# Kernel optimization log

Hardware: AMD Instinct MI355X
Metric: run time of the kernel (lower is better)

## Reference

```python
import jax, jax.numpy as jnp
import numpy as np

BN_EPS = 1e-5


def setup_inputs() -> dict:
    key = jax.random.key(0)
    ks = jax.random.split(key, 12)
    B, N, G, D = 16, 8192, 64, 384
    C_IN = D + 64 + 3  # 451
    inp = {
        "features": jax.random.normal(ks[0], (B, G, D), jnp.float32),
        "centers": jax.random.normal(ks[1], (B, G, 3), jnp.float32),
        "pc": jax.random.normal(ks[2], (B, N, 3), jnp.float32),
        "category": jax.random.randint(ks[3], (B,), 0, 16, jnp.int64),
        "cat_embed": jax.random.normal(ks[4], (16, 64), jnp.float32) * 0.02,
        "w1": jax.random.normal(ks[5], (256, C_IN), jnp.float32) * (1.0 / np.sqrt(C_IN)),
        "b1": jnp.zeros((256,), jnp.float32),
        "g1": jnp.ones((256,), jnp.float32),
        "be1": jnp.zeros((256,), jnp.float32),
        "m1": jnp.zeros((256,), jnp.float32),
        "v1": jnp.ones((256,), jnp.float32),
        "w2": jax.random.normal(ks[6], (256, 256), jnp.float32) * (1.0 / 16.0),
        "b2": jnp.zeros((256,), jnp.float32),
        "g2": jnp.ones((256,), jnp.float32),
        "be2": jnp.zeros((256,), jnp.float32),
        "m2": jnp.zeros((256,), jnp.float32),
        "v2": jnp.ones((256,), jnp.float32),
        "w3": jax.random.normal(ks[7], (50, 256), jnp.float32) * (1.0 / 16.0),
        "b3": jnp.zeros((50,), jnp.float32),
    }
    return inp


def _bn(x, g, be, m, v):  # x: [B, N, C], inference-mode BatchNorm1d
    return (x - m) * (g * jax.lax.rsqrt(v + BN_EPS)) + be


def reference(features, centers, pc, category, cat_embed,
              w1, b1, g1, be1, m1, v1,
              w2, b2, g2, be2, m2, v2,
              w3, b3):
    B, N, _ = pc.shape
    # Euclidean cdist via norm expansion: [B, N, G]
    p2 = jnp.sum(pc * pc, axis=-1, keepdims=True)            # [B,N,1]
    c2 = jnp.sum(centers * centers, axis=-1)[:, None, :]     # [B,1,G]
    dot = jnp.einsum('bnd,bgd->bng', pc, centers)
    dist = jnp.sqrt(jnp.clip(p2 + c2 - 2.0 * dot, 1e-12))
    # top-3 smallest
    neg_d, knn_idx = jax.lax.top_k(-dist, 3)                 # [B,N,3]
    knn_dist = -neg_d
    w = 1.0 / (knn_dist + 1e-8)
    w = w / jnp.sum(w, axis=-1, keepdims=True)               # [B,N,3]
    # gather per-batch: features [B,G,D], knn_idx [B,N,3] -> [B,N,3,D]
    knn_features = jax.vmap(lambda f, i: f[i])(features, knn_idx)
    point_features = jnp.einsum('bnkd,bnk->bnd', knn_features, w)  # [B,N,D]
    cat_feat = jnp.broadcast_to(cat_embed[category][:, None, :], (B, N, 64))
    combined = jnp.concatenate([point_features, cat_feat, pc], axis=-1)  # [B,N,451]
    # Conv1d(k=1) == per-point dense layer; keep [B,N,C] layout
    h = jnp.einsum('bnc,oc->bno', combined, w1) + b1
    h = jax.nn.relu(_bn(h, g1, be1, m1, v1))
    h = jnp.einsum('bnc,oc->bno', h, w2) + b2
    h = jax.nn.relu(_bn(h, g2, be2, m2, v2))
    seg_logits = jnp.einsum('bnc,oc->bno', h, w3) + b3       # [B,N,50]
    return seg_logits
```

## Files before the change

### kernel.cpp

```cpp
#include <hip/hip_runtime.h>

#define TPB 256

typedef unsigned short u16;
typedef unsigned int u32;
typedef short short8 __attribute__((ext_vector_type(8)));
typedef float f32x4 __attribute__((ext_vector_type(4)));

#define KEEP(x) asm volatile("" :: "v"(x))
#define PIN(x)  asm volatile("" : "+v"(x))

__device__ __forceinline__ u16 f2bf(float x) {
  union { float f; u32 u; } v;
  v.f = x;
  u32 r = v.u + 0x7FFFu + ((v.u >> 16) & 1u);
  return (u16)(r >> 16);
}

__device__ __forceinline__ float bf2f(u16 x) {
  union { u32 u; float f; } v;
  v.u = ((u32)x) << 16;
  return v.f;
}

__global__ void prep_kernel(const float* __restrict__ w1, const float* __restrict__ b1,
                            const float* __restrict__ g1, const float* __restrict__ be1,
                            const float* __restrict__ m1, const float* __restrict__ v1,
                            const float* __restrict__ w2, const float* __restrict__ b2,
                            const float* __restrict__ g2, const float* __restrict__ be2,
                            const float* __restrict__ m2, const float* __restrict__ v2,
                            const float* __restrict__ w3, const float* __restrict__ b3,
                            const float* __restrict__ features,
                            u16* __restrict__ w1b, u16* __restrict__ w2b, u16* __restrict__ w3b,
                            float* __restrict__ b1p, float* __restrict__ b2p, float* __restrict__ b3p,
                            u16* __restrict__ Fbf)
{
  int i = blockIdx.x * TPB + threadIdx.x;
  if (i < 256 * 480) {
    int o = i / 480;
    int k = i - o * 480;
    float s = g1[o] * rsqrtf(v1[o] + 1e-5f);
    u16 r = 0;
    if (k < 451) r = f2bf(w1[o * 451 + k] * s);
    w1b[i] = r;
  }
  if (i < 256 * 256) {
    int o = i >> 8;
    float s = g2[o] * rsqrtf(v2[o] + 1e-5f);
    w2b[i] = f2bf(w2[i] * s);
  }
  if (i < 64 * 256) {
    int o = i >> 8;
    u16 r = 0;
    if (o < 50) r = f2bf(w3[i]);
    w3b[i] = r;
  }
  if (i < 256) {
    float s1 = g1[i] * rsqrtf(v1[i] + 1e-5f);
    b1p[i] = (b1[i] - m1[i]) * s1 + be1[i];
    float s2 = g2[i] * rsqrtf(v2[i] + 1e-5f);
    b2p[i] = (b2[i] - m2[i]) * s2 + be2[i];
  }
  if (i < 64) {
    b3p[i] = (i < 50) ? b3[i] : 0.f;
  }
  if (i < 98304) {
    f32x4 v = ((const f32x4*)features)[i];
    u32 lo = (u32)f2bf(v[0]) | ((u32)f2bf(v[1]) << 16);
    u32 hi = (u32)f2bf(v[2]) | ((u32)f2bf(v[3]) << 16);
    *(uint2*)&Fbf[i * 4] = make_uint2(lo, hi);
  }
}

__global__ __launch_bounds__(256, 8)
void gcalc_kernel(const u16* __restrict__ Fbf, const int* __restrict__ category,
                  const float* __restrict__ cat_embed, const u16* __restrict__ w1b,
                  const float* __restrict__ b1p,
                  u16* __restrict__ G, float* __restrict__ bias1)
{
  const int b    = blockIdx.x >> 4;
  const int og   = blockIdx.x & 15;
  const int tid  = threadIdx.x;
  const int lane = tid & 63;
  const int wv   = tid >> 6;
  const int lr   = lane & 15;
  const int lk   = (lane >> 4) * 8;
  const int r0   = (lane >> 4) * 4;
  const u16* Fb  = Fbf + b * 24576;
  const int ch   = og * 16 + lr;

  f32x4 acc = {0.f, 0.f, 0.f, 0.f};
  #pragma unroll
  for (int ks = 0; ks < 12; ++ks) {
    short8 av = *(const short8*)(Fb + (wv * 16 + lr) * 384 + ks * 32 + lk);
    short8 bv = *(const short8*)(w1b + ch * 480 + ks * 32 + lk);
    acc = __builtin_amdgcn_mfma_f32_16x16x32_bf16(av, bv, acc, 0, 0, 0);
  }
  #pragma unroll
  for (int r = 0; r < 4; ++r)
    G[(b * 256 + ch) * 96 + wv * 16 + r0 + r] = f2bf(acc[r]);

  if (tid < 16) {
    int o = og * 16 + tid;
    const u16* wr = w1b + o * 480 + 384;
    const float* ce = cat_embed + category[b] * 64;
    float a = b1p[o];
    #pragma unroll 8
    for (int j = 0; j < 64; ++j) a += bf2f(wr[j]) * ce[j];
    bias1[b * 256 + o] = a;
    u16* Go = G + (b * 256 + o) * 96;
    Go[64] = wr[64]; Go[65] = wr[65]; Go[66] = wr[66];
    #pragma unroll
    for (int k = 67; k < 96; ++k) Go[k] = 0;
  }
}

#define LDP 104
#define LDH 264

__global__ __launch_bounds__(512, 4)
void fused_kernel(const float* __restrict__ centers, const float* __restrict__ pc,
                  const u16* __restrict__ G, const float* __restrict__ bias1,
                  const u16* __restrict__ w2b, const u16* __restrict__ w3b,
                  const float* __restrict__ b2p, const float* __restrict__ b3p,
                  float* __restrict__ out)
{
  __shared__ u16 hbuf[128 * LDH];
  __shared__ float centl[192];
  __shared__ float pcl[384];

  const int bx   = blockIdx.x;
  const int b    = bx >> 6;
  const int n0   = (bx & 63) << 7;
  const int tid  = threadIdx.x;
  const int lane = tid & 63;
  const int wv   = tid >> 6;
  const int lr   = lane & 15;
  const int lk   = (lane >> 4) * 8;
  const int r0   = (lane >> 4) * 4;

  u16*   Pm   = hbuf;
  float* scrd = (float*)((char*)hbuf + 32768);
  int*   scri = (int*)((char*)hbuf + 40960);

  short8 bvG[3][2];
  #pragma unroll
  for (int ks = 0; ks < 3; ++ks)
    #pragma unroll
    for (int n = 0; n < 2; ++n)
      bvG[ks][n] = *(const short8*)(G + (b * 256 + wv * 32 + n * 16 + lr) * 96 + ks * 32 + lk);

  {
    u32* Pw = (u32*)Pm;
    #pragma unroll
    for (int i = 0; i < 13; ++i) Pw[tid + 512 * i] = 0;
  }
  if (tid < 192) centl[tid] = centers[b * 192 + tid];
  if (tid < 384) pcl[tid] = pc[(b * 8192 + n0) * 3 + tid];
  __syncthreads();

  {
    int p = tid >> 2, c = tid & 3;
    float px = pcl[p * 3 + 0], py = pcl[p * 3 + 1], pz = pcl[p * 3 + 2];
    float p2 = px * px + py * py + pz * pz;
    float bd0 = 3.4e38f, bd1 = 3.4e38f, bd2 = 3.4e38f;
    int bi0 = 0, bi1 = 0, bi2 = 0;
    int j0 = c * 16;
    for (int j = j0; j < j0 + 16; ++j) {
      float cx = centl[j * 3 + 0], cy = centl[j * 3 + 1], cz = centl[j * 3 + 2];
      float dotv = px * cx + py * cy + pz * cz;
      float c2 = cx * cx + cy * cy + cz * cz;
      float d2 = (p2 + c2) - 2.f * dotv;
      if (d2 < bd2) {
        if (d2 < bd1) {
          if (d2 < bd0) { bd2 = bd1; bi2 = bi1; bd1 = bd0; bi1 = bi0; bd0 = d2; bi0 = j; }
          else          { bd2 = bd1; bi2 = bi1; bd1 = d2; bi1 = j; }
        } else          { bd2 = d2; bi2 = j; }
      }
    }
    scrd[tid * 3 + 0] = bd0; scrd[tid * 3 + 1] = bd1; scrd[tid * 3 + 2] = bd2;
    scri[tid * 3 + 0] = bi0; scri[tid * 3 + 1] = bi1; scri[tid * 3 + 2] = bi2;
  }
  __syncthreads();

  if (tid < 128) {
    float bd0 = 3.4e38f, bd1 = 3.4e38f, bd2 = 3.4e38f;
    int bi0 = 0, bi1 = 0, bi2 = 0;
    #pragma unroll
    for (int c = 0; c < 4; ++c) {
      int t = tid * 4 + c;
      #pragma unroll
      for (int s = 0; s < 3; ++s) {
        float d2 = scrd[t * 3 + s];
        int   j  = scri[t * 3 + s];
        if (d2 < bd2) {
          if (d2 < bd1) {
            if (d2 < bd0) { bd2 = bd1; bi2 = bi1; bd1 = bd0; bi1 = bi0; bd0 = d2; bi0 = j; }
            else          { bd2 = bd1; bi2 = bi1; bd1 = d2; bi1 = j; }
          } else          { bd2 = d2; bi2 = j; }
        }
      }
    }
    float dd0 = sqrtf(fmaxf(bd0, 1e-12f));
    float dd1 = sqrtf(fmaxf(bd1, 1e-12f));
    float dd2 = sqrtf(fmaxf(bd2, 1e-12f));
    float u0 = 1.f / (dd0 + 1e-8f);
    float u1 = 1.f / (dd1 + 1e-8f);
    float u2 = 1.f / (dd2 + 1e-8f);
    float inv = 1.f / (u0 + u1 + u2);
    u16* Pr = Pm + tid * LDP;
    Pr[bi0] = f2bf(u0 * inv);
    Pr[bi1] = f2bf(u1 * inv);
    Pr[bi2] = f2bf(u2 * inv);
    Pr[64] = f2bf(pcl[tid * 3 + 0]);
    Pr[65] = f2bf(pcl[tid * 3 + 1]);
    Pr[66] = f2bf(pcl[tid * 3 + 2]);
  }
  KEEP(bvG[0][0]); KEEP(bvG[0][1]); KEEP(bvG[1][0]);
  KEEP(bvG[1][1]); KEEP(bvG[2][0]); KEEP(bvG[2][1]);
  __syncthreads();
  PIN(bvG[0][0]); PIN(bvG[0][1]); PIN(bvG[1][0]);
  PIN(bvG[1][1]); PIN(bvG[2][0]); PIN(bvG[2][1]);

  f32x4 acc[8][2];
  {
    f32x4 z = {0.f, 0.f, 0.f, 0.f};
    #pragma unroll
    for (int m = 0; m < 8; ++m) { acc[m][0] = z; acc[m][1] = z; }
  }
  #pragma unroll
  for (int ks = 0; ks < 3; ++ks) {
    short8 av[8];
    #pragma unroll
    for (int m = 0; m < 8; ++m)
      av[m] = *(const short8*)(&Pm[(m * 16 + lr) * LDP + ks * 32 + lk]);
    #pragma unroll
    for (int m = 0; m < 8; ++m)
      #pragma unroll
      for (int n = 0; n < 2; ++n)
        acc[m][n] = __builtin_amdgcn_mfma_f32_16x16x32_bf16(av[m], bvG[ks][n], acc[m][n], 0, 0, 0);
  }
  __syncthreads();

  #pragma unroll
  for (int n = 0; n < 2; ++n) {
    float bb = bias1[b * 256 + wv * 32 + n * 16 + lr];
    #pragma unroll
    for (int m = 0; m < 8; ++m)
      #pragma unroll
      for (int r = 0; r < 4; ++r) {
        float v = acc[m][n][r] + bb;
        v = v > 0.f ? v : 0.f;
        int row = m * 16 + r0 + r;
        int col = (wv * 32 + n * 16 + lr) ^ (((row >> 2) & 7) << 3);
        hbuf[row * LDH + col] = f2bf(v);
      }
  }

  short8 w2f[2][2];
  #pragma unroll
  for (int ks = 0; ks < 2; ++ks)
    #pragma unroll
    for (int n = 0; n < 2; ++n)
      w2f[ks][n] = *(const short8*)(w2b + (wv * 32 + n * 16 + lr) * 256 + ks * 32 + lk);
  KEEP(w2f[0][0]); KEEP(w2f[0][1]); KEEP(w2f[1][0]); KEEP(w2f[1][1]);
  __syncthreads();
  PIN(w2f[0][0]); PIN(w2f[0][1]); PIN(w2f[1][0]); PIN(w2f[1][1]);

  {
    f32x4 z = {0.f, 0.f, 0.f, 0.f};
    #pragma unroll
    for (int m = 0; m < 8; ++m) { acc[m][0] = z; acc[m][1] = z; }
  }
  #pragma unroll
  for (int ks = 0; ks < 8; ++ks) {
    short8 bv[2];
    if (ks < 2) { bv[0] = w2f[ks][0]; bv[1] = w2f[ks][1]; }
    else {
      #pragma unroll
      for (int n = 0; n < 2; ++n)
        bv[n] = *(const short8*)(w2b + (wv * 32 + n * 16 + lr) * 256 + ks * 32 + lk);
    }
    short8 av[8];
    #pragma unroll
    for (int m = 0; m < 8; ++m) {
      int row = m * 16 + lr;
      int g = (ks * 4 + (lane >> 4)) ^ ((row >> 2) & 7);
      av[m] = *(const short8*)(&hbuf[row * LDH + g * 8]);
    }
    #pragma unroll
    for (int m = 0; m < 8; ++m)
      #pragma unroll
      for (int n = 0; n < 2; ++n)
        acc[m][n] = __builtin_amdgcn_mfma_f32_16x16x32_bf16(av[m], bv[n], acc[m][n], 0, 0, 0);
  }
  __syncthreads();

  #pragma unroll
  for (int n = 0; n < 2; ++n) {
    float bb = b2p[wv * 32 + n * 16 + lr];
    #pragma unroll
    for (int m = 0; m < 8; ++m)
      #pragma unroll
      for (int r = 0; r < 4; ++r) {
        float v = acc[m][n][r] + bb;
        v = v > 0.f ? v : 0.f;
        int row = m * 16 + r0 + r;
        int col = (wv * 32 + n * 16 + lr) ^ (((row >> 2) & 7) << 3);
        hbuf[row * LDH + col] = f2bf(v);
      }
  }

  const int wm = wv & 3;
  const int wn = wv >> 2;
  short8 w3f[8][2];
  #pragma unroll
  for (int ks = 0; ks < 8; ++ks)
    #pragma unroll
    for (int j = 0; j < 2; ++j)
      w3f[ks][j] = *(const short8*)(w3b + (wn * 32 + j * 16 + lr) * 256 + ks * 32 + lk);
  #pragma unroll
  for (int ks = 0; ks < 8; ++ks) { KEEP(w3f[ks][0]); KEEP(w3f[ks][1]); }
  __syncthreads();
  #pragma unroll
  for (int ks = 0; ks < 8; ++ks) { PIN(w3f[ks][0]); PIN(w3f[ks][1]); }

  f32x4 acc3[2][2];
  {
    f32x4 z = {0.f, 0.f, 0.f, 0.f};
    acc3[0][0] = z; acc3[0][1] = z; acc3[1][0] = z; acc3[1][1] = z;
  }
  #pragma unroll
  for (int ks = 0; ks < 8; ++ks) {
    #pragma unroll
    for (int mi = 0; mi < 2; ++mi) {
      int row = (wm * 2 + mi) * 16 + lr;
      int g = (ks * 4 + (lane >> 4)) ^ ((row >> 2) & 7);
      short8 av = *(const short8*)(&hbuf[row * LDH + g * 8]);
      #pragma unroll
      for (int j = 0; j < 2; ++j)
        acc3[mi][j] = __builtin_amdgcn_mfma_f32_16x16x32_bf16(av, w3f[ks][j], acc3[mi][j], 0, 0, 0);
    }
  }
  __syncthreads();

  {
    float* logb = (float*)hbuf;
    #pragma unroll
    for (int j = 0; j < 2; ++j) {
      int c = wn * 32 + j * 16 + lr;
      if (c < 50) {
        float b3v = b3p[c];
        #pragma unroll
        for (int mi = 0; mi < 2; ++mi)
          #pragma unroll
          for (int r = 0; r < 4; ++r) {
            int row = (wm * 2 + mi) * 16 + r0 + r;
            logb[row * 52 + c] = acc3[mi][j][r] + b3v;
          }
      }
    }
    __syncthreads();
    float* outb = out + (size_t)(b * 8192 + n0) * 50;
    #pragma unroll
    for (int i = 0; i < 13; ++i) {
      int f = tid + i * 512;
      if (f < 6400) {
        int row = (f * 5243) >> 18;
        int c = f - row * 50;
        outb[f] = logb[row * 52 + c];
      }
    }
  }
}

extern "C" void kernel_launch(void* const* d_in, const int* in_sizes, int n_in,
                              void* d_out, int out_size, void* d_ws, size_t ws_size,
                              hipStream_t stream) {
  const float* features  = (const float*)d_in[0];
  const float* centers   = (const float*)d_in[1];
  const float* pc        = (const float*)d_in[2];
  const int*   category  = (const int*)d_in[3];
  const float* cat_embed = (const float*)d_in[4];
  const float* w1  = (const float*)d_in[5];
  const float* b1  = (const float*)d_in[6];
  const float* g1  = (const float*)d_in[7];
  const float* be1 = (const float*)d_in[8];
  const float* m1  = (const float*)d_in[9];
  const float* v1  = (const float*)d_in[10];
  const float* w2  = (const float*)d_in[11];
  const float* b2  = (const float*)d_in[12];
  const float* g2  = (const float*)d_in[13];
  const float* be2 = (const float*)d_in[14];
  const float* m2  = (const float*)d_in[15];
  const float* v2  = (const float*)d_in[16];
  const float* w3  = (const float*)d_in[17];
  const float* b3  = (const float*)d_in[18];
  float* out = (float*)d_out;

  char* ws = (char*)d_ws;
  u16*   w1b   = (u16*)(ws);
  u16*   w2b   = (u16*)(ws + 245760);
  u16*   w3b   = (u16*)(ws + 376832);
  float* b1p   = (float*)(ws + 409600);
  float* b2p   = (float*)(ws + 410624);
  float* b3p   = (float*)(ws + 411648);
  u16*   G     = (u16*)(ws + 412672);
  float* bias1 = (float*)(ws + 1199104);
  u16*   Fbf   = (u16*)(ws + 1215488);

  prep_kernel<<<480, TPB, 0, stream>>>(w1, b1, g1, be1, m1, v1,
                                       w2, b2, g2, be2, m2, v2,
                                       w3, b3, features,
                                       w1b, w2b, w3b, b1p, b2p, b3p, Fbf);
  gcalc_kernel<<<256, 256, 0, stream>>>(Fbf, category, cat_embed, w1b, b1p, G, bias1);

  fused_kernel<<<1024, 512, 0, stream>>>(centers, pc, G, bias1,
                                         w2b, w3b, b2p, b3p, out);
}
```

Measured before the change: 167.3 us.

## Halve fused-kernel tile to 64 points with 4 waves and direct output stores

The fused MLP kernel now processes 64 points per block with 256 threads instead of 128 points with 512 threads, and launches twice as many blocks. Each wave covers 64 output channels across 4 row tiles, so the warp tile is reshaped from 8x2 to 4x4 MFMA fragments. The register prefetching of G/w2 fragments across barriers is removed, the swizzle pattern is changed with an unpadded LDS stride, and logits are written straight to global memory instead of being staged through LDS for coalesced stores. The intent is smaller LDS use and more resident blocks. The cost is more weight reloads per point and uncoalesced strided output writes.

```diff
diff --git a/kernel.cpp b/kernel.cpp
--- a/kernel.cpp
+++ b/kernel.cpp
@@ -8,7 +8,6 @@
 typedef float f32x4 __attribute__((ext_vector_type(4)));
 
 #define KEEP(x) asm volatile("" :: "v"(x))
-#define PIN(x)  asm volatile("" : "+v"(x))
 
 __device__ __forceinline__ u16 f2bf(float x) {
   union { float f; u32 u; } v;
@@ -116,22 +115,22 @@
 }
 
 #define LDP 104
-#define LDH 264
-
-__global__ __launch_bounds__(512, 4)
+#define LDH 256
+
+__global__ __launch_bounds__(256, 4)
 void fused_kernel(const float* __restrict__ centers, const float* __restrict__ pc,
                   const u16* __restrict__ G, const float* __restrict__ bias1,
                   const u16* __restrict__ w2b, const u16* __restrict__ w3b,
                   const float* __restrict__ b2p, const float* __restrict__ b3p,
                   float* __restrict__ out)
 {
-  __shared__ u16 hbuf[128 * LDH];
+  __shared__ u16 hbuf[64 * LDH];
   __shared__ float centl[192];
-  __shared__ float pcl[384];
+  __shared__ float pcl[192];
 
   const int bx   = blockIdx.x;
-  const int b    = bx >> 6;
-  const int n0   = (bx & 63) << 7;
+  const int b    = bx >> 7;
+  const int n0   = (bx & 127) << 6;
   const int tid  = threadIdx.x;
   const int lane = tid & 63;
   const int wv   = tid >> 6;
@@ -140,23 +139,18 @@
   const int r0   = (lane >> 4) * 4;
 
   u16*   Pm   = hbuf;
-  float* scrd = (float*)((char*)hbuf + 32768);
-  int*   scri = (int*)((char*)hbuf + 40960);
-
-  short8 bvG[3][2];
-  #pragma unroll
-  for (int ks = 0; ks < 3; ++ks)
-    #pragma unroll
-    for (int n = 0; n < 2; ++n)
-      bvG[ks][n] = *(const short8*)(G + (b * 256 + wv * 32 + n * 16 + lr) * 96 + ks * 32 + lk);
+  float* scrd = (float*)((char*)hbuf + 16384);
+  int*   scri = (int*)((char*)hbuf + 19456);
 
   {
     u32* Pw = (u32*)Pm;
     #pragma unroll
-    for (int i = 0; i < 13; ++i) Pw[tid + 512 * i] = 0;
-  }
-  if (tid < 192) centl[tid] = centers[b * 192 + tid];
-  if (tid < 384) pcl[tid] = pc[(b * 8192 + n0) * 3 + tid];
+    for (int i = 0; i < 13; ++i) Pw[tid + 256 * i] = 0;
+  }
+  if (tid < 192) {
+    centl[tid] = centers[b * 192 + tid];
+    pcl[tid]   = pc[(b * 8192 + n0) * 3 + tid];
+  }
   __syncthreads();
 
   {
@@ -183,7 +177,7 @@
   }
   __syncthreads();
 
-  if (tid < 128) {
+  if (tid < 64) {
     float bd0 = 3.4e38f, bd1 = 3.4e38f, bd2 = 3.4e38f;
     int bi0 = 0, bi1 = 0, bi2 = 0;
     #pragma unroll
@@ -216,160 +210,124 @@
     Pr[65] = f2bf(pcl[tid * 3 + 1]);
     Pr[66] = f2bf(pcl[tid * 3 + 2]);
   }
-  KEEP(bvG[0][0]); KEEP(bvG[0][1]); KEEP(bvG[1][0]);
-  KEEP(bvG[1][1]); KEEP(bvG[2][0]); KEEP(bvG[2][1]);
-  __syncthreads();
-  PIN(bvG[0][0]); PIN(bvG[0][1]); PIN(bvG[1][0]);
-  PIN(bvG[1][1]); PIN(bvG[2][0]); PIN(bvG[2][1]);
-
-  f32x4 acc[8][2];
+  __syncthreads();
+
+  f32x4 acc[4][4];
   {
     f32x4 z = {0.f, 0.f, 0.f, 0.f};
     #pragma unroll
-    for (int m = 0; m < 8; ++m) { acc[m][0] = z; acc[m][1] = z; }
+    for (int m = 0; m < 4; ++m)
+      #pragma unroll
+      for (int n = 0; n < 4; ++n) acc[m][n] = z;
   }
   #pragma unroll
   for (int ks = 0; ks < 3; ++ks) {
-    short8 av[8];
-    #pragma unroll
-    for (int m = 0; m < 8; ++m)
+    short8 av[4], bv[4];
+    #pragma unroll
+    for (int m = 0; m < 4; ++m)
       av[m] = *(const short8*)(&Pm[(m * 16 + lr) * LDP + ks * 32 + lk]);
     #pragma unroll
-    for (int m = 0; m < 8; ++m)
-      #pragma unroll
-      for (int n = 0; n < 2; ++n)
-        acc[m][n] = __builtin_amdgcn_mfma_f32_16x16x32_bf16(av[m], bvG[ks][n], acc[m][n], 0, 0, 0);
-  }
-  __syncthreads();
-
-  #pragma unroll
-  for (int n = 0; n < 2; ++n) {
-    float bb = bias1[b * 256 + wv * 32 + n * 16 + lr];
-    #pragma unroll
-    for (int m = 0; m < 8; ++m)
+    for (int n = 0; n < 4; ++n)
+      bv[n] = *(const short8*)(G + (b * 256 + wv * 64 + n * 16 + lr) * 96 + ks * 32 + lk);
+    #pragma unroll
+    for (int m = 0; m < 4; ++m)
+      #pragma unroll
+      for (int n = 0; n < 4; ++n)
+        acc[m][n] = __builtin_amdgcn_mfma_f32_16x16x32_bf16(av[m], bv[n], acc[m][n], 0, 0, 0);
+  }
+  __syncthreads();
+
+  #pragma unroll
+  for (int n = 0; n < 4; ++n) {
+    float bb = bias1[b * 256 + wv * 64 + n * 16 + lr];
+    #pragma unroll
+    for (int m = 0; m < 4; ++m)
       #pragma unroll
       for (int r = 0; r < 4; ++r) {
         float v = acc[m][n][r] + bb;
         v = v > 0.f ? v : 0.f;
         int row = m * 16 + r0 + r;
-        int col = (wv * 32 + n * 16 + lr) ^ (((row >> 2) & 7) << 3);
+        int col = (wv * 64 + n * 16 + lr) ^ ((row & 7) << 3);
         hbuf[row * LDH + col] = f2bf(v);
       }
   }
-
-  short8 w2f[2][2];
-  #pragma unroll
-  for (int ks = 0; ks < 2; ++ks)
-    #pragma unroll
-    for (int n = 0; n < 2; ++n)
-      w2f[ks][n] = *(const short8*)(w2b + (wv * 32 + n * 16 + lr) * 256 + ks * 32 + lk);
-  KEEP(w2f[0][0]); KEEP(w2f[0][1]); KEEP(w2f[1][0]); KEEP(w2f[1][1]);
-  __syncthreads();
-  PIN(w2f[0][0]); PIN(w2f[0][1]); PIN(w2f[1][0]); PIN(w2f[1][1]);
+  __syncthreads();
 
   {
     f32x4 z = {0.f, 0.f, 0.f, 0.f};
     #pragma unroll
-    for (int m = 0; m < 8; ++m) { acc[m][0] = z; acc[m][1] = z; }
+    for (int m = 0; m < 4; ++m)
+      #pragma unroll
+      for (int n = 0; n < 4; ++n) acc[m][n] = z;
   }
   #pragma unroll
   for (int ks = 0; ks < 8; ++ks) {
-    short8 bv[2];
-    if (ks < 2) { bv[0] = w2f[ks][0]; bv[1] = w2f[ks][1]; }
-    else {
-      #pragma unroll
-      for (int n = 0; n < 2; ++n)
-        bv[n] = *(const short8*)(w2b + (wv * 32 + n * 16 + lr) * 256 + ks * 32 + lk);
-    }
-    short8 av[8];
-    #pragma unroll
-    for (int m = 0; m < 8; ++m) {
+    short8 bv[4], av[4];
+    #pragma unroll
+    for (int n = 0; n < 4; ++n)
+      bv[n] = *(const short8*)(w2b + (wv * 64 + n * 16 + lr) * 256 + ks * 32 + lk);
+    #pragma unroll
+    for (int m = 0; m < 4; ++m) {
       int row = m * 16 + lr;
-      int g = (ks * 4 + (lane >> 4)) ^ ((row >> 2) & 7);
+      int g = (ks * 4 + (lane >> 4)) ^ (row & 7);
       av[m] = *(const short8*)(&hbuf[row * LDH + g * 8]);
     }
     #pragma unroll
-    for (int m = 0; m < 8; ++m)
-      #pragma unroll
-      for (int n = 0; n < 2; ++n)
+    for (int m = 0; m < 4; ++m)
+      #pragma unroll
+      for (int n = 0; n < 4; ++n)
         acc[m][n] = __builtin_amdgcn_mfma_f32_16x16x32_bf16(av[m], bv[n], acc[m][n], 0, 0, 0);
   }
   __syncthreads();
 
   #pragma unroll
-  for (int n = 0; n < 2; ++n) {
-    float bb = b2p[wv * 32 + n * 16 + lr];
-    #pragma unroll
-    for (int m = 0; m < 8; ++m)
+  for (int n = 0; n < 4; ++n) {
+    float bb = b2p[wv * 64 + n * 16 + lr];
+    #pragma unroll
+    for (int m = 0; m < 4; ++m)
       #pragma unroll
       for (int r = 0; r < 4; ++r) {
         float v = acc[m][n][r] + bb;
         v = v > 0.f ? v : 0.f;
         int row = m * 16 + r0 + r;
-        int col = (wv * 32 + n * 16 + lr) ^ (((row >> 2) & 7) << 3);
+        int col = (wv * 64 + n * 16 + lr) ^ ((row & 7) << 3);
         hbuf[row * LDH + col] = f2bf(v);
       }
   }
 
-  const int wm = wv & 3;
-  const int wn = wv >> 2;
-  short8 w3f[8][2];
+  short8 w3f[8];
   #pragma unroll
   for (int ks = 0; ks < 8; ++ks)
-    #pragma unroll
-    for (int j = 0; j < 2; ++j)
-      w3f[ks][j] = *(const short8*)(w3b + (wn * 32 + j * 16 + lr) * 256 + ks * 32 + lk);
-  #pragma unroll
-  for (int ks = 0; ks < 8; ++ks) { KEEP(w3f[ks][0]); KEEP(w3f[ks][1]); }
-  __syncthreads();
-  #pragma unroll
-  for (int ks = 0; ks < 8; ++ks) { PIN(w3f[ks][0]); PIN(w3f[ks][1]); }
-
-  f32x4 acc3[2][2];
-  {
+    w3f[ks] = *(const short8*)(w3b + (wv * 16 + lr) * 256 + ks * 32 + lk);
+  #pragma unroll
+  for (int ks = 0; ks < 8; ++ks) KEEP(w3f[ks]);
+  __syncthreads();
+
+  {
+    f32x4 acc3[4];
     f32x4 z = {0.f, 0.f, 0.f, 0.f};
-    acc3[0][0] = z; acc3[0][1] = z; acc3[1][0] = z; acc3[1][1] = z;
-  }
-  #pragma unroll
-  for (int ks = 0; ks < 8; ++ks) {
-    #pragma unroll
-    for (int mi = 0; mi < 2; ++mi) {
-      int row = (wm * 2 + mi) * 16 + lr;
-      int g = (ks * 4 + (lane >> 4)) ^ ((row >> 2) & 7);
-      short8 av = *(const short8*)(&hbuf[row * LDH + g * 8]);
-      #pragma unroll
-      for (int j = 0; j < 2; ++j)
-        acc3[mi][j] = __builtin_amdgcn_mfma_f32_16x16x32_bf16(av, w3f[ks][j], acc3[mi][j], 0, 0, 0);
-    }
-  }
-  __syncthreads();
-
-  {
-    float* logb = (float*)hbuf;
-    #pragma unroll
-    for (int j = 0; j < 2; ++j) {
-      int c = wn * 32 + j * 16 + lr;
-      if (c < 50) {
-        float b3v = b3p[c];
+    #pragma unroll
+    for (int m = 0; m < 4; ++m) acc3[m] = z;
+    #pragma unroll
+    for (int ks = 0; ks < 8; ++ks) {
+      #pragma unroll
+      for (int m = 0; m < 4; ++m) {
+        int row = m * 16 + lr;
+        int g = (ks * 4 + (lane >> 4)) ^ (row & 7);
+        short8 av = *(const short8*)(&hbuf[row * LDH + g * 8]);
+        acc3[m] = __builtin_amdgcn_mfma_f32_16x16x32_bf16(av, w3f[ks], acc3[m], 0, 0, 0);
+      }
+    }
+    int c = wv * 16 + lr;
+    if (c < 50) {
+      float b3v = b3p[c];
+      #pragma unroll
+      for (int m = 0; m < 4; ++m)
         #pragma unroll
-        for (int mi = 0; mi < 2; ++mi)
-          #pragma unroll
-          for (int r = 0; r < 4; ++r) {
-            int row = (wm * 2 + mi) * 16 + r0 + r;
-            logb[row * 52 + c] = acc3[mi][j][r] + b3v;
-          }
-      }
-    }
-    __syncthreads();
-    float* outb = out + (size_t)(b * 8192 + n0) * 50;
-    #pragma unroll
-    for (int i = 0; i < 13; ++i) {
-      int f = tid + i * 512;
-      if (f < 6400) {
-        int row = (f * 5243) >> 18;
-        int c = f - row * 50;
-        outb[f] = logb[row * 52 + c];
-      }
+        for (int r = 0; r < 4; ++r) {
+          int row = n0 + m * 16 + r0 + r;
+          out[(b * 8192 + row) * 50 + c] = acc3[m][r] + b3v;
+        }
     }
   }
 }
@@ -415,6 +373,6 @@
                                        w1b, w2b, w3b, b1p, b2p, b3p, Fbf);
   gcalc_kernel<<<256, 256, 0, stream>>>(Fbf, category, cat_embed, w1b, b1p, G, bias1);
 
-  fused_kernel<<<1024, 512, 0, stream>>>(centers, pc, G, bias1,
+  fused_kernel<<<2048, 256, 0, stream>>>(centers, pc, G, bias1,
                                          w2b, w3b, b2p, b3p, out);
 }
```

New measurement: 190.8 us. 14.0% more time.
